# Kernel tuning notes

Measured on AMD Instinct MI355X. Metric: run time of the kernel, lower is better.

Reference implementation:

```python
import jax, jax.numpy as jnp
import numpy as np

H_IN, H_CELL, L = 1342, 256, 3
B, T = 128, 128


def _gru_bias(key, n3, scale, h):
    b = jax.random.uniform(key, (n3,), jnp.float32, -scale, scale)
    # PyTorch init hack in the module: bias[n//4:n//2] = 1.0 (n = 3*H_cell)
    return b.at[n3 // 4: n3 // 2].set(1.0)


def setup_inputs() -> dict:
    key = jax.random.key(0)
    ks = jax.random.split(key, 4 * L + 4)
    inp = {}
    inp["OpAdj_hs_history"] = jax.random.normal(ks[0], (B, T, H_IN), jnp.float32)
    inp["hidden"] = jax.random.normal(ks[1], (L, B, H_CELL), jnp.float32)
    s = 1.0 / np.sqrt(H_CELL)
    n3 = 3 * H_CELL
    for l in range(L):
        in_dim = H_IN if l == 0 else H_CELL
        k0, k1, k2, k3 = jax.random.split(ks[2 + l], 4)
        inp[f"w_ih_{l}"] = jax.random.uniform(k0, (n3, in_dim), jnp.float32, -s, s)
        inp[f"w_hh_{l}"] = jax.random.uniform(k1, (n3, H_CELL), jnp.float32, -s, s)
        inp[f"b_ih_{l}"] = _gru_bias(k2, n3, s, H_CELL)
        inp[f"b_hh_{l}"] = _gru_bias(k3, n3, s, H_CELL)
    sf = 1.0 / np.sqrt(L * H_CELL)
    inp["fc_w"] = jax.random.uniform(ks[2 + L], (H_IN, L * H_CELL), jnp.float32, -sf, sf)
    inp["fc_b"] = jax.random.uniform(ks[3 + L], (H_IN,), jnp.float32, -sf, sf)
    return inp


def _gru_layer(xs, h0, w_ih, w_hh, b_ih, b_hh):
    # xs: (T, B, in_dim); precompute input projections for all timesteps
    gx = jnp.einsum('tbi,gi->tbg', xs, w_ih) + b_ih  # (T, B, 3H)

    def step(h, gx_t):
        gh = h @ w_hh.T + b_hh                      # (B, 3H)
        xr, xz, xn = jnp.split(gx_t, 3, axis=-1)
        hr, hz, hn = jnp.split(gh, 3, axis=-1)
        r = jax.nn.sigmoid(xr + hr)
        z = jax.nn.sigmoid(xz + hz)
        n = jnp.tanh(xn + r * hn)
        h_new = (1.0 - z) * n + z * h
        return h_new, h_new

    hT, ys = jax.lax.scan(step, h0, gx)
    return ys, hT


def reference(OpAdj_hs_history, hidden,
              w_ih_0, w_hh_0, b_ih_0, b_hh_0,
              w_ih_1, w_hh_1, b_ih_1, b_hh_1,
              w_ih_2, w_hh_2, b_ih_2, b_hh_2,
              fc_w, fc_b):
    params = [(w_ih_0, w_hh_0, b_ih_0, b_hh_0),
              (w_ih_1, w_hh_1, b_ih_1, b_hh_1),
              (w_ih_2, w_hh_2, b_ih_2, b_hh_2)]
    xs = jnp.transpose(OpAdj_hs_history, (1, 0, 2))  # (T, B, H_in)
    finals = []
    for l in range(L):
        xs, hT = _gru_layer(xs, hidden[l], *params[l])
        finals.append(hT)
    hn = jnp.stack(finals, axis=0)                   # (L, B, H)
    hn_flat = jnp.transpose(hn, (1, 0, 2)).reshape(-1, L * H_CELL)
    out = (hn_flat @ fc_w.T + fc_b).reshape(-1, 1, H_IN)
    return out, hidden
```

## Files before the change

kernel.cpp:

```cpp
#include <hip/hip_runtime.h>
#include <hip/hip_bf16.h>

typedef __bf16 bf16;
typedef _Float16 fp16;
typedef __attribute__((ext_vector_type(8))) __bf16 bf16x8;
typedef __attribute__((ext_vector_type(4))) __bf16 bf16x4;
typedef __attribute__((ext_vector_type(4))) _Float16 fp16x4;
typedef __attribute__((ext_vector_type(4))) float f32x4;
typedef __attribute__((ext_vector_type(4))) unsigned int u32x4;
typedef long long i64;

#define H_IN 1342
#define TT   128
#define BB   128

static __device__ __forceinline__ f32x4 mfma16(bf16x8 a, bf16x8 b, f32x4 c) {
    return __builtin_amdgcn_mfma_f32_16x16x32_bf16(a, b, c, 0, 0, 0);
}
static __device__ __forceinline__ f32x4 mfma8(i64 a, i64 b, f32x4 c) {
    return __builtin_amdgcn_mfma_f32_16x16x32_fp8_fp8(a, b, c, 0, 0, 0);
}

static __device__ __forceinline__ float fexp2(float x) {
#if __has_builtin(__builtin_amdgcn_exp2f)
    return __builtin_amdgcn_exp2f(x);
#else
    float r; asm("v_exp_f32 %0, %1" : "=v"(r) : "v"(x)); return r;
#endif
}
static __device__ __forceinline__ float frcp(float x) {
#if __has_builtin(__builtin_amdgcn_rcpf)
    return __builtin_amdgcn_rcpf(x);
#else
    float r; asm("v_rcp_f32 %0, %1" : "=v"(r) : "v"(x)); return r;
#endif
}
static __device__ __forceinline__ float sigf(float x) {
    return frcp(1.f + fexp2(x * -1.44269504f));
}
static __device__ __forceinline__ float tanhfast(float x) {
    return __builtin_fmaf(2.f, frcp(1.f + fexp2(x * -2.88539008f)), -1.f);
}

static __device__ __forceinline__ unsigned char f2e4m3(float x) {
    unsigned char sgn = (unsigned char)((__builtin_bit_cast(unsigned int, x) >> 24) & 0x80);
    float ax = fabsf(x);
    if (ax < 0.015625f) {
        float q = nearbyintf(ax * 512.f);
        return sgn | (unsigned char)(int)q;
    }
    if (ax >= 448.f) return sgn | 0x7E;
    int e; float m = frexpf(ax, &e);
    float q = nearbyintf(m * 16.f);
    int E = e - 1;
    if (q == 16.f) { q = 8.f; E += 1; }
    if (E > 8) return sgn | 0x7E;
    return sgn | (unsigned char)((E + 7) << 3) | (unsigned char)((int)q & 7);
}

static __device__ __forceinline__ unsigned int pk_fp8(float a, float b) {
#if __has_builtin(__builtin_amdgcn_cvt_pk_fp8_f32)
    return (unsigned int)__builtin_amdgcn_cvt_pk_fp8_f32(a, b, 0, false);
#else
    unsigned int r;
    asm("v_cvt_pk_fp8_f32 %0, %1, %2" : "=v"(r) : "v"(a), "v"(b));
    return r;
#endif
}

__global__ void prep_pack2(const float* __restrict__ whh0,
                           const float* __restrict__ whh1,
                           const float* __restrict__ whh2,
                           unsigned char* __restrict__ Wh8)
{
    int idx = blockIdx.x * blockDim.x + threadIdx.x;
    if (idx < 589824) {
        int l = idx / 196608;
        int r = idx - l * 196608;
        const float* w = (l == 0) ? whh0 : (l == 1) ? whh1 : whh2;
        int f = r >> 9, q = r & 511;
        int lane = q >> 3, j = q & 7;
        int nt = f >> 3, kt = f & 7;
        int n = nt * 16 + (lane & 15);
        int k = kt * 32 + (lane >> 4) * 8 + j;
        Wh8[idx] = f2e4m3(w[n * 256 + k]);
    }
}

__global__ __launch_bounds__(512) void gemm_gx0(const float* __restrict__ X,
                                                const float* __restrict__ W,
                                                const float* __restrict__ bih,
                                                const float* __restrict__ bhh,
                                                char*  __restrict__ gxt)
{
    __shared__ bf16 As[128][40];
    __shared__ bf16 Bs[256][40];
    const int tid  = threadIdx.x;
    const int lane = tid & 63;
    const int w    = tid >> 6;
    const int cl   = lane & 15;
    const int lh   = lane >> 4;
    const int n0   = blockIdx.y * 256;

    f32x4 acc[16];
#pragma unroll
    for (int i = 0; i < 16; ++i) acc[i] = (f32x4){0.f, 0.f, 0.f, 0.f};

    for (int kt = 0; kt < 42; ++kt) {
        const int k0 = kt * 32;
        {
            int row = tid >> 2;
            int c   = (tid & 3) * 8;
            const float* src = X + ((size_t)row * 128 + blockIdx.x) * H_IN + (k0 + c);
            bf16x8 pk;
            if (k0 + c + 8 <= H_IN) {
                const float2* s2 = (const float2*)src;
                float2 v0 = s2[0], v1 = s2[1], v2 = s2[2], v3 = s2[3];
                pk[0] = (bf16)v0.x; pk[1] = (bf16)v0.y; pk[2] = (bf16)v1.x; pk[3] = (bf16)v1.y;
                pk[4] = (bf16)v2.x; pk[5] = (bf16)v2.y; pk[6] = (bf16)v3.x; pk[7] = (bf16)v3.y;
            } else {
#pragma unroll
                for (int i = 0; i < 8; ++i)
                    pk[i] = (bf16)((k0 + c + i < H_IN) ? src[i] : 0.f);
            }
            *(bf16x8*)&As[row][c] = pk;
        }
        {
            int row = tid >> 1;
            int c   = (tid & 1) * 16;
            const float* src = W + (size_t)(n0 + row) * H_IN + (k0 + c);
#pragma unroll
            for (int h = 0; h < 2; ++h) {
                const float* s = src + h * 8;
                bf16x8 pk;
                if (k0 + c + h * 8 + 8 <= H_IN) {
                    const float2* s2 = (const float2*)s;
                    float2 v0 = s2[0], v1 = s2[1], v2 = s2[2], v3 = s2[3];
                    pk[0] = (bf16)v0.x; pk[1] = (bf16)v0.y; pk[2] = (bf16)v1.x; pk[3] = (bf16)v1.y;
                    pk[4] = (bf16)v2.x; pk[5] = (bf16)v2.y; pk[6] = (bf16)v3.x; pk[7] = (bf16)v3.y;
                } else {
#pragma unroll
                    for (int i = 0; i < 8; ++i)
                        pk[i] = (bf16)((k0 + c + h * 8 + i < H_IN) ? s[i] : 0.f);
                }
                *(bf16x8*)&Bs[row][c + h * 8] = pk;
            }
        }
        __syncthreads();
        bf16x8 a = *(const bf16x8*)&As[w * 16 + cl][lh * 8];
#pragma unroll
        for (int nt = 0; nt < 16; ++nt) {
            bf16x8 b = *(const bf16x8*)&Bs[nt * 16 + cl][lh * 8];
            acc[nt] = mfma16(a, b, acc[nt]);
        }
        __syncthreads();
    }
    char* base = gxt + (((size_t)blockIdx.x * 8 + w) << 15);
#pragma unroll
    for (int nt = 0; nt < 16; ++nt) {
        const int col = n0 + nt * 16 + cl;
        if (col < 256) {
            fp16x4 pk;
#pragma unroll
            for (int r = 0; r < 4; ++r) pk[r] = (fp16)(acc[nt][r] + bih[col] + bhh[col]);
            *(fp16x4*)(base + col * 32 + 8 * lh) = pk;
        } else if (col < 512) {
            fp16x4 pk;
#pragma unroll
            for (int r = 0; r < 4; ++r) pk[r] = (fp16)(acc[nt][r] + bih[col] + bhh[col]);
            *(fp16x4*)(base + 8192 + (col - 256) * 32 + 8 * lh) = pk;
        } else {
            float4 pk = {acc[nt][0] + bih[col], acc[nt][1] + bih[col],
                         acc[nt][2] + bih[col], acc[nt][3] + bih[col]};
            *(float4*)(base + 16384 + (col - 512) * 64 + 16 * lh) = pk;
        }
    }
}

__global__ __launch_bounds__(512) void gemm_gxy(const bf16* __restrict__ Y,
                                                const float* __restrict__ W,
                                                const float* __restrict__ bih,
                                                const float* __restrict__ bhh,
                                                char*  __restrict__ gxt)
{
    __shared__ bf16 As[128][40];
    __shared__ bf16 Bs[256][40];
    const int tid  = threadIdx.x;
    const int lane = tid & 63;
    const int w    = tid >> 6;
    const int cl   = lane & 15;
    const int lh   = lane >> 4;
    const int rm0  = blockIdx.x * 128;
    const int n0   = blockIdx.y * 256;

    f32x4 acc[16];
#pragma unroll
    for (int i = 0; i < 16; ++i) acc[i] = (f32x4){0.f, 0.f, 0.f, 0.f};

    for (int kt = 0; kt < 8; ++kt) {
        const int k0 = kt * 32;
        {
            int row = tid >> 2;
            int c   = (tid & 3) * 8;
            *(bf16x8*)&As[row][c] =
                *(const bf16x8*)(Y + (size_t)(rm0 + row) * 256 + k0 + c);
        }
        {
            int row = tid >> 1;
            int c   = (tid & 1) * 16;
            const float* src = W + (size_t)(n0 + row) * 256 + (k0 + c);
#pragma unroll
            for (int h = 0; h < 2; ++h) {
                const float2* s2 = (const float2*)(src + h * 8);
                float2 v0 = s2[0], v1 = s2[1], v2 = s2[2], v3 = s2[3];
                bf16x8 pk;
                pk[0] = (bf16)v0.x; pk[1] = (bf16)v0.y; pk[2] = (bf16)v1.x; pk[3] = (bf16)v1.y;
                pk[4] = (bf16)v2.x; pk[5] = (bf16)v2.y; pk[6] = (bf16)v3.x; pk[7] = (bf16)v3.y;
                *(bf16x8*)&Bs[row][c + h * 8] = pk;
            }
        }
        __syncthreads();
        bf16x8 a = *(const bf16x8*)&As[w * 16 + cl][lh * 8];
#pragma unroll
        for (int nt = 0; nt < 16; ++nt) {
            bf16x8 b = *(const bf16x8*)&Bs[nt * 16 + cl][lh * 8];
            acc[nt] = mfma16(a, b, acc[nt]);
        }
        __syncthreads();
    }
    char* base = gxt + (((size_t)blockIdx.x * 8 + w) << 15);
#pragma unroll
    for (int nt = 0; nt < 16; ++nt) {
        const int col = n0 + nt * 16 + cl;
        if (col < 256) {
            fp16x4 pk;
#pragma unroll
            for (int r = 0; r < 4; ++r) pk[r] = (fp16)(acc[nt][r] + bih[col] + bhh[col]);
            *(fp16x4*)(base + col * 32 + 8 * lh) = pk;
        } else if (col < 512) {
            fp16x4 pk;
#pragma unroll
            for (int r = 0; r < 4; ++r) pk[r] = (fp16)(acc[nt][r] + bih[col] + bhh[col]);
            *(fp16x4*)(base + 8192 + (col - 256) * 32 + 8 * lh) = pk;
        } else {
            float4 pk = {acc[nt][0] + bih[col], acc[nt][1] + bih[col],
                         acc[nt][2] + bih[col], acc[nt][3] + bih[col]};
            *(float4*)(base + 16384 + (col - 512) * 64 + 16 * lh) = pk;
        }
    }
}

__global__ __launch_bounds__(1024)
void gru_rec(
    const char* __restrict__ gxt,
    const unsigned char* __restrict__ Wh8,
    const float* __restrict__ bhh,
    const float* __restrict__ h0,
    bf16*  __restrict__ Y,
    float* __restrict__ hnfL)
{
    __shared__ unsigned char WL[131072];
    __shared__ unsigned char Ah8[2][16][264];
    __shared__ bf16 Yst[2][16][264];

    const int tid  = threadIdx.x;
    const int lane = tid & 63;
    const int w    = tid >> 6;
    const int cl   = lane & 15;
    const int lh   = lane >> 4;
    const int g    = blockIdx.x;
    const int col  = 16 * w + cl;

#pragma unroll
    for (int i = 0; i < 8; ++i) {
        const int off = (tid + i * 1024) * 16;
        *(u32x4*)&WL[off] = *(const u32x4*)(Wh8 + off);
    }
    const float bN = bhh[512 + col];

    float hprev[4];
#pragma unroll
    for (int r = 0; r < 4; ++r) {
        const int m = 4 * lh + r;
        float v = h0[(size_t)(g * 16 + m) * 256 + col];
        hprev[r] = v;
        Ah8[1][m][col] = f2e4m3(v);
    }
    __syncthreads();

    for (int t = 0; t < TT; ++t) {
        const int slot = t & 1;
        const int rb   = (t + 1) & 1;

        if (t > 0) {
            const int yrow = tid >> 6;
            const int yc   = (tid & 63) * 4;
            bf16x4 yv = *(const bf16x4*)&Yst[(t - 1) & 1][yrow][yc];
            *(bf16x4*)(Y + ((size_t)(t - 1) * BB + g * 16 + yrow) * 256 + yc) = yv;
        }

        const char* gt = gxt + (((size_t)t * 8 + g) << 15);
        fp16x4 rv = *(const fp16x4*)(gt + col * 32 + 8 * lh);
        fp16x4 zv = *(const fp16x4*)(gt + 8192 + col * 32 + 8 * lh);
        f32x4  nv = *(const f32x4*) (gt + 16384 + col * 64 + 16 * lh);
        i64 Bn[8];
#pragma unroll
        for (int kk = 0; kk < 8; ++kk)
            Bn[kk] = *(const i64*)(Wh8 + (size_t)(((32 + w) * 8 + kk) * 512) + lane * 8);

        f32x4 cr = (f32x4){0.f,0.f,0.f,0.f};
        f32x4 cz = (f32x4){0.f,0.f,0.f,0.f};
        f32x4 cn = (f32x4){0.f,0.f,0.f,0.f};
        i64 areg[8];
        __builtin_amdgcn_s_setprio(1);
#pragma unroll
        for (int kk = 0; kk < 8; ++kk) {
            i64 a = *(const i64*)&Ah8[rb][cl][kk * 32 + lh * 8];
            areg[kk] = a;
            cr = mfma8(a, *(const i64*)&WL[(size_t)(( w       * 8 + kk) * 512) + lane * 8], cr);
            cz = mfma8(a, *(const i64*)&WL[(size_t)(((16 + w) * 8 + kk) * 512) + lane * 8], cz);
        }
#pragma unroll
        for (int kk = 0; kk < 8; ++kk)
            cn = mfma8(areg[kk], Bn[kk], cn);
        __builtin_amdgcn_s_setprio(0);

        float hn4[4];
#pragma unroll
        for (int r = 0; r < 4; ++r) {
            const int m = 4 * lh + r;
            float rr_ = sigf((float)rv[r] + cr[r]);
            float zz  = sigf((float)zv[r] + cz[r]);
            float nn  = tanhfast(__builtin_fmaf(rr_, cn[r] + bN, nv[r]));
            float hnew = __builtin_fmaf(zz, hprev[r] - nn, nn);
            hprev[r] = hnew;
            hn4[r] = hnew;
            Yst[slot][m][col] = (bf16)hnew;
        }
        {
            unsigned int p0 = pk_fp8(hn4[0], hn4[1]);
            unsigned int p1 = pk_fp8(hn4[2], hn4[3]);
            const int m0 = 4 * lh;
            Ah8[slot][m0 + 0][col] = (unsigned char)(p0 & 0xff);
            Ah8[slot][m0 + 1][col] = (unsigned char)((p0 >> 8) & 0xff);
            Ah8[slot][m0 + 2][col] = (unsigned char)(p1 & 0xff);
            Ah8[slot][m0 + 3][col] = (unsigned char)((p1 >> 8) & 0xff);
        }

        asm volatile("s_waitcnt lgkmcnt(0)" ::: "memory");
        __builtin_amdgcn_sched_barrier(0);
        __builtin_amdgcn_s_barrier();
        __builtin_amdgcn_sched_barrier(0);
    }

#pragma unroll
    for (int r = 0; r < 4; ++r) {
        const int m = 4 * lh + r;
        hnfL[(size_t)(g * 16 + m) * 768 + col] = hprev[r];
    }
    {
        const int yrow = tid >> 6;
        const int yc   = (tid & 63) * 4;
        bf16x4 yv = *(const bf16x4*)&Yst[(TT - 1) & 1][yrow][yc];
        *(bf16x4*)(Y + ((size_t)(TT - 1) * BB + g * 16 + yrow) * 256 + yc) = yv;
    }
}

__global__ __launch_bounds__(512) void fc_gemm(const float* __restrict__ hn,
                                               const float* __restrict__ fcw,
                                               const float* __restrict__ fcb,
                                               float* __restrict__ out)
{
    __shared__ bf16 As[128][40];
    __shared__ bf16 Bs[256][40];
    const int tid  = threadIdx.x;
    const int lane = tid & 63;
    const int w    = tid >> 6;
    const int cl   = lane & 15;
    const int lh   = lane >> 4;
    const int n0   = blockIdx.x * 256;

    f32x4 acc[16];
#pragma unroll
    for (int i = 0; i < 16; ++i) acc[i] = (f32x4){0.f, 0.f, 0.f, 0.f};

    for (int kt = 0; kt < 24; ++kt) {
        const int k0 = kt * 32;
        {
            int row = tid >> 2;
            int c   = (tid & 3) * 8;
            const float2* s2 = (const float2*)(hn + (size_t)row * 768 + k0 + c);
            float2 v0 = s2[0], v1 = s2[1], v2 = s2[2], v3 = s2[3];
            bf16x8 pk;
            pk[0] = (bf16)v0.x; pk[1] = (bf16)v0.y; pk[2] = (bf16)v1.x; pk[3] = (bf16)v1.y;
            pk[4] = (bf16)v2.x; pk[5] = (bf16)v2.y; pk[6] = (bf16)v3.x; pk[7] = (bf16)v3.y;
            *(bf16x8*)&As[row][c] = pk;
        }
        {
            int row = tid >> 1;
            int c   = (tid & 1) * 16;
            const int n = n0 + row;
#pragma unroll
            for (int h = 0; h < 2; ++h) {
                bf16x8 pk;
                if (n < H_IN) {
                    const float2* s2 = (const float2*)(fcw + (size_t)n * 768 + k0 + c + h * 8);
                    float2 v0 = s2[0], v1 = s2[1], v2 = s2[2], v3 = s2[3];
                    pk[0] = (bf16)v0.x; pk[1] = (bf16)v0.y; pk[2] = (bf16)v1.x; pk[3] = (bf16)v1.y;
                    pk[4] = (bf16)v2.x; pk[5] = (bf16)v2.y; pk[6] = (bf16)v3.x; pk[7] = (bf16)v3.y;
                } else {
#pragma unroll
                    for (int i = 0; i < 8; ++i) pk[i] = (bf16)0.f;
                }
                *(bf16x8*)&Bs[row][c + h * 8] = pk;
            }
        }
        __syncthreads();
        bf16x8 a = *(const bf16x8*)&As[w * 16 + cl][lh * 8];
#pragma unroll
        for (int nt = 0; nt < 16; ++nt) {
            bf16x8 b = *(const bf16x8*)&Bs[nt * 16 + cl][lh * 8];
            acc[nt] = mfma16(a, b, acc[nt]);
        }
        __syncthreads();
    }
#pragma unroll
    for (int nt = 0; nt < 16; ++nt) {
#pragma unroll
        for (int r = 0; r < 4; ++r) {
            int b   = w * 16 + 4 * lh + r;
            int col = n0 + nt * 16 + cl;
            if (col < H_IN)
                out[(size_t)b * H_IN + col] = acc[nt][r] + fcb[col];
        }
    }
}

extern "C" void kernel_launch(void* const* d_in, const int* in_sizes, int n_in,
                              void* d_out, int out_size, void* d_ws, size_t ws_size,
                              hipStream_t stream) {
    const float* X    = (const float*)d_in[0];
    const float* hid  = (const float*)d_in[1];
    const float* wih0 = (const float*)d_in[2];
    const float* whh0 = (const float*)d_in[3];
    const float* bih0 = (const float*)d_in[4];
    const float* bhh0 = (const float*)d_in[5];
    const float* wih1 = (const float*)d_in[6];
    const float* whh1 = (const float*)d_in[7];
    const float* bih1 = (const float*)d_in[8];
    const float* bhh1 = (const float*)d_in[9];
    const float* wih2 = (const float*)d_in[10];
    const float* whh2 = (const float*)d_in[11];
    const float* bih2 = (const float*)d_in[12];
    const float* bhh2 = (const float*)d_in[13];
    const float* fcw  = (const float*)d_in[14];
    const float* fcb  = (const float*)d_in[15];
    float* out = (float*)d_out;

    char* ws = (char*)d_ws;
    unsigned char* Wh8 = (unsigned char*)ws;
    float* hnf   = (float*)(ws + 1188864);
    bf16*  Y     = (bf16*)(ws + 1582080);
    char*  gxt   = ws + 9970688;

    prep_pack2<<<dim3(1152), dim3(512), 0, stream>>>(whh0, whh1, whh2, Wh8);
    gemm_gx0<<<dim3(128, 3), dim3(512), 0, stream>>>(X, wih0, bih0, bhh0, gxt);
    gru_rec<<<dim3(8), dim3(1024), 0, stream>>>(gxt, Wh8, bhh0, hid, Y, hnf);
    gemm_gxy<<<dim3(128, 3), dim3(512), 0, stream>>>(Y, wih1, bih1, bhh1, gxt);
    gru_rec<<<dim3(8), dim3(1024), 0, stream>>>(gxt, Wh8 + 196608, bhh1,
                                                hid + 32768, Y, hnf + 256);
    gemm_gxy<<<dim3(128, 3), dim3(512), 0, stream>>>(Y, wih2, bih2, bhh2, gxt);
    gru_rec<<<dim3(8), dim3(1024), 0, stream>>>(gxt, Wh8 + 393216, bhh2,
                                                hid + 65536, Y, hnf + 512);
    fc_gemm<<<dim3(6), dim3(512), 0, stream>>>(hnf, fcw, fcb, out);
    hipMemcpyAsync(out + 171776, hid, 98304 * sizeof(float),
                   hipMemcpyDeviceToDevice, stream);
}
```

Measured before the change: 770.6 us.

## Pre-convert input weights to bf16 once and reorder recurrent-step MFMA before Y store

Extends the weight prep kernel to also convert w_ih for all three layers into padded bf16 buffers, so the input-projection GEMMs load bf16 directly instead of re-reading fp32 and converting in every block. This is meant to cut global traffic and conversion ALU work in gemm_gx0/gemm_gxy, at the cost of a larger prep kernel and a bigger workspace. Separately, the recurrent loop moves the gx loads and the MFMA chain ahead of the previous-step Y store and adds unroll 2, with the aim of putting the critical-path matmul earlier in each step.

```diff
diff --git a/kernel.cpp b/kernel.cpp
--- a/kernel.cpp
+++ b/kernel.cpp
@@ -68,10 +68,16 @@
 #endif
 }
 
-__global__ void prep_pack2(const float* __restrict__ whh0,
+__global__ void prep_pack3(const float* __restrict__ whh0,
                            const float* __restrict__ whh1,
                            const float* __restrict__ whh2,
-                           unsigned char* __restrict__ Wh8)
+                           const float* __restrict__ wih0,
+                           const float* __restrict__ wih1,
+                           const float* __restrict__ wih2,
+                           unsigned char* __restrict__ Wh8,
+                           bf16* __restrict__ Wb0,
+                           bf16* __restrict__ Wb1,
+                           bf16* __restrict__ Wb2)
 {
     int idx = blockIdx.x * blockDim.x + threadIdx.x;
     if (idx < 589824) {
@@ -84,11 +90,21 @@
         int n = nt * 16 + (lane & 15);
         int k = kt * 32 + (lane >> 4) * 8 + j;
         Wh8[idx] = f2e4m3(w[n * 256 + k]);
+    } else if (idx < 589824 + 1032192) {
+        int i = idx - 589824;
+        int n = i / 1344, k = i - n * 1344;
+        Wb0[i] = (k < H_IN) ? (bf16)wih0[(size_t)n * H_IN + k] : (bf16)0.f;
+    } else if (idx < 589824 + 1032192 + 196608) {
+        int i = idx - (589824 + 1032192);
+        Wb1[i] = (bf16)wih1[i];
+    } else if (idx < 2015232) {
+        int i = idx - (589824 + 1032192 + 196608);
+        Wb2[i] = (bf16)wih2[i];
     }
 }
 
 __global__ __launch_bounds__(512) void gemm_gx0(const float* __restrict__ X,
-                                                const float* __restrict__ W,
+                                                const bf16* __restrict__ Wb,
                                                 const float* __restrict__ bih,
                                                 const float* __restrict__ bhh,
                                                 char*  __restrict__ gxt)
@@ -128,23 +144,9 @@
         {
             int row = tid >> 1;
             int c   = (tid & 1) * 16;
-            const float* src = W + (size_t)(n0 + row) * H_IN + (k0 + c);
-#pragma unroll
-            for (int h = 0; h < 2; ++h) {
-                const float* s = src + h * 8;
-                bf16x8 pk;
-                if (k0 + c + h * 8 + 8 <= H_IN) {
-                    const float2* s2 = (const float2*)s;
-                    float2 v0 = s2[0], v1 = s2[1], v2 = s2[2], v3 = s2[3];
-                    pk[0] = (bf16)v0.x; pk[1] = (bf16)v0.y; pk[2] = (bf16)v1.x; pk[3] = (bf16)v1.y;
-                    pk[4] = (bf16)v2.x; pk[5] = (bf16)v2.y; pk[6] = (bf16)v3.x; pk[7] = (bf16)v3.y;
-                } else {
-#pragma unroll
-                    for (int i = 0; i < 8; ++i)
-                        pk[i] = (bf16)((k0 + c + h * 8 + i < H_IN) ? s[i] : 0.f);
-                }
-                *(bf16x8*)&Bs[row][c + h * 8] = pk;
-            }
+            const bf16* src = Wb + (size_t)(n0 + row) * 1344 + k0 + c;
+            *(bf16x8*)&Bs[row][c]     = ((const bf16x8*)src)[0];
+            *(bf16x8*)&Bs[row][c + 8] = ((const bf16x8*)src)[1];
         }
         __syncthreads();
         bf16x8 a = *(const bf16x8*)&As[w * 16 + cl][lh * 8];
@@ -178,7 +180,7 @@
 }
 
 __global__ __launch_bounds__(512) void gemm_gxy(const bf16* __restrict__ Y,
-                                                const float* __restrict__ W,
+                                                const bf16* __restrict__ Wb,
                                                 const float* __restrict__ bih,
                                                 const float* __restrict__ bhh,
                                                 char*  __restrict__ gxt)
@@ -208,16 +210,9 @@
         {
             int row = tid >> 1;
             int c   = (tid & 1) * 16;
-            const float* src = W + (size_t)(n0 + row) * 256 + (k0 + c);
-#pragma unroll
-            for (int h = 0; h < 2; ++h) {
-                const float2* s2 = (const float2*)(src + h * 8);
-                float2 v0 = s2[0], v1 = s2[1], v2 = s2[2], v3 = s2[3];
-                bf16x8 pk;
-                pk[0] = (bf16)v0.x; pk[1] = (bf16)v0.y; pk[2] = (bf16)v1.x; pk[3] = (bf16)v1.y;
-                pk[4] = (bf16)v2.x; pk[5] = (bf16)v2.y; pk[6] = (bf16)v3.x; pk[7] = (bf16)v3.y;
-                *(bf16x8*)&Bs[row][c + h * 8] = pk;
-            }
+            const bf16* src = Wb + (size_t)(n0 + row) * 256 + k0 + c;
+            *(bf16x8*)&Bs[row][c]     = ((const bf16x8*)src)[0];
+            *(bf16x8*)&Bs[row][c + 8] = ((const bf16x8*)src)[1];
         }
         __syncthreads();
         bf16x8 a = *(const bf16x8*)&As[w * 16 + cl][lh * 8];
@@ -288,9 +283,36 @@
     }
     __syncthreads();
 
+#pragma unroll 2
     for (int t = 0; t < TT; ++t) {
         const int slot = t & 1;
         const int rb   = (t + 1) & 1;
+
+        const char* gt = gxt + (((size_t)t * 8 + g) << 15);
+        fp16x4 rv = *(const fp16x4*)(gt + col * 32 + 8 * lh);
+        fp16x4 zv = *(const fp16x4*)(gt + 8192 + col * 32 + 8 * lh);
+        f32x4  nv = *(const f32x4*) (gt + 16384 + col * 64 + 16 * lh);
+        i64 Bn[8];
+#pragma unroll
+        for (int kk = 0; kk < 8; ++kk)
+            Bn[kk] = *(const i64*)(Wh8 + (size_t)(((32 + w) * 8 + kk) * 512) + lane * 8);
+
+        f32x4 cr = (f32x4){0.f,0.f,0.f,0.f};
+        f32x4 cz = (f32x4){0.f,0.f,0.f,0.f};
+        f32x4 cn = (f32x4){0.f,0.f,0.f,0.f};
+        i64 areg[8];
+        __builtin_amdgcn_s_setprio(1);
+#pragma unroll
+        for (int kk = 0; kk < 8; ++kk) {
+            i64 a = *(const i64*)&Ah8[rb][cl][kk * 32 + lh * 8];
+            areg[kk] = a;
+            cr = mfma8(a, *(const i64*)&WL[(size_t)(( w       * 8 + kk) * 512) + lane * 8], cr);
+            cz = mfma8(a, *(const i64*)&WL[(size_t)(((16 + w) * 8 + kk) * 512) + lane * 8], cz);
+        }
+#pragma unroll
+        for (int kk = 0; kk < 8; ++kk)
+            cn = mfma8(areg[kk], Bn[kk], cn);
+        __builtin_amdgcn_s_setprio(0);
 
         if (t > 0) {
             const int yrow = tid >> 6;
@@ -298,32 +320,6 @@
             bf16x4 yv = *(const bf16x4*)&Yst[(t - 1) & 1][yrow][yc];
             *(bf16x4*)(Y + ((size_t)(t - 1) * BB + g * 16 + yrow) * 256 + yc) = yv;
         }
-
-        const char* gt = gxt + (((size_t)t * 8 + g) << 15);
-        fp16x4 rv = *(const fp16x4*)(gt + col * 32 + 8 * lh);
-        fp16x4 zv = *(const fp16x4*)(gt + 8192 + col * 32 + 8 * lh);
-        f32x4  nv = *(const f32x4*) (gt + 16384 + col * 64 + 16 * lh);
-        i64 Bn[8];
-#pragma unroll
-        for (int kk = 0; kk < 8; ++kk)
-            Bn[kk] = *(const i64*)(Wh8 + (size_t)(((32 + w) * 8 + kk) * 512) + lane * 8);
-
-        f32x4 cr = (f32x4){0.f,0.f,0.f,0.f};
-        f32x4 cz = (f32x4){0.f,0.f,0.f,0.f};
-        f32x4 cn = (f32x4){0.f,0.f,0.f,0.f};
-        i64 areg[8];
-        __builtin_amdgcn_s_setprio(1);
-#pragma unroll
-        for (int kk = 0; kk < 8; ++kk) {
-            i64 a = *(const i64*)&Ah8[rb][cl][kk * 32 + lh * 8];
-            areg[kk] = a;
-            cr = mfma8(a, *(const i64*)&WL[(size_t)(( w       * 8 + kk) * 512) + lane * 8], cr);
-            cz = mfma8(a, *(const i64*)&WL[(size_t)(((16 + w) * 8 + kk) * 512) + lane * 8], cz);
-        }
-#pragma unroll
-        for (int kk = 0; kk < 8; ++kk)
-            cn = mfma8(areg[kk], Bn[kk], cn);
-        __builtin_amdgcn_s_setprio(0);
 
         float hn4[4];
 #pragma unroll
@@ -459,17 +455,22 @@
 
     char* ws = (char*)d_ws;
     unsigned char* Wh8 = (unsigned char*)ws;
-    float* hnf   = (float*)(ws + 1188864);
-    bf16*  Y     = (bf16*)(ws + 1582080);
-    char*  gxt   = ws + 9970688;
-
-    prep_pack2<<<dim3(1152), dim3(512), 0, stream>>>(whh0, whh1, whh2, Wh8);
-    gemm_gx0<<<dim3(128, 3), dim3(512), 0, stream>>>(X, wih0, bih0, bhh0, gxt);
+    bf16*  Wb0  = (bf16*)(ws + 589824);
+    bf16*  Wb1  = (bf16*)(ws + 2654208);
+    bf16*  Wb2  = (bf16*)(ws + 3047424);
+    float* hnf  = (float*)(ws + 3440640);
+    bf16*  Y    = (bf16*)(ws + 3833856);
+    char*  gxt  = ws + 12222464;
+
+    prep_pack3<<<dim3(3936), dim3(512), 0, stream>>>(whh0, whh1, whh2,
+                                                     wih0, wih1, wih2,
+                                                     Wh8, Wb0, Wb1, Wb2);
+    gemm_gx0<<<dim3(128, 3), dim3(512), 0, stream>>>(X, Wb0, bih0, bhh0, gxt);
     gru_rec<<<dim3(8), dim3(1024), 0, stream>>>(gxt, Wh8, bhh0, hid, Y, hnf);
-    gemm_gxy<<<dim3(128, 3), dim3(512), 0, stream>>>(Y, wih1, bih1, bhh1, gxt);
+    gemm_gxy<<<dim3(128, 3), dim3(512), 0, stream>>>(Y, Wb1, bih1, bhh1, gxt);
     gru_rec<<<dim3(8), dim3(1024), 0, stream>>>(gxt, Wh8 + 196608, bhh1,
                                                 hid + 32768, Y, hnf + 256);
-    gemm_gxy<<<dim3(128, 3), dim3(512), 0, stream>>>(Y, wih2, bih2, bhh2, gxt);
+    gemm_gxy<<<dim3(128, 3), dim3(512), 0, stream>>>(Y, Wb2, bih2, bhh2, gxt);
     gru_rec<<<dim3(8), dim3(1024), 0, stream>>>(gxt, Wh8 + 393216, bhh2,
                                                 hid + 65536, Y, hnf + 512);
     fc_gemm<<<dim3(6), dim3(512), 0, stream>>>(hnf, fcw, fcb, out);
```

Measured after the change: 764.7 us. No clear change (-0.8%).
